# Kernel tuning notes

Hardware: AMD Instinct MI355X
Metric: run time of the kernel (lower is better)

Reference implementation:

```python
import jax, jax.numpy as jnp
import numpy as np

TEMPERATURE = 0.15
SINKHORN_ITERS = 5
CHUNKS = 8
DIM = 4096
CHUNK_SIZE = DIM // CHUNKS


def _sinkhorn(logits, num_iters=SINKHORN_ITERS):
    # Alternating row (dim=-1) then column (dim=-2) log-normalization, matching torch order.
    log_p = logits
    for _ in range(num_iters):
        log_p = log_p - jax.nn.logsumexp(log_p, axis=-1, keepdims=True)
        log_p = log_p - jax.nn.logsumexp(log_p, axis=-2, keepdims=True)
    return jnp.exp(log_p)


def setup_inputs() -> dict:
    key = jax.random.key(0)
    k1, k2, k3 = jax.random.split(key, 3)
    x = jax.random.normal(k1, (4, 4096, DIM), dtype=jnp.float32)
    chunk_logits = 0.01 * jax.random.normal(k2, (CHUNKS, CHUNKS), dtype=jnp.float32)
    intra_logits = 0.01 * jax.random.normal(k3, (CHUNKS, CHUNK_SIZE, CHUNK_SIZE), dtype=jnp.float32)
    return {"x": x, "chunk_logits": chunk_logits, "intra_logits": intra_logits}


def reference(x, chunk_logits, intra_logits):
    orig_shape = x.shape
    y = x.reshape(-1, CHUNKS, CHUNK_SIZE)  # [B, c, d]
    chunk_perm = _sinkhorn(chunk_logits / TEMPERATURE)  # [c, c]
    y = jnp.einsum('ij,bjd->bid', chunk_perm, y)
    intra_perm = _sinkhorn(intra_logits / TEMPERATURE)  # [c, d, d]
    # out[b,c,k] = sum_j y[b,c,j] * intra_perm[c,k,j]  (y @ intra_perm^T per chunk)
    y = jnp.einsum('bcj,ckj->bck', y, intra_perm)
    return y.reshape(orig_shape)
```

## Files before the change

kernel.cpp:

```cpp
#include <hip/hip_runtime.h>
#include <cstdint>
#include <cstddef>

typedef unsigned short u16;
typedef __bf16 bf16x8 __attribute__((ext_vector_type(8)));
typedef float f32x4 __attribute__((ext_vector_type(4)));
typedef u16 u16x8 __attribute__((ext_vector_type(8)));

typedef const void __attribute__((address_space(1)))* gas_ptr;
typedef void __attribute__((address_space(3)))* las_ptr;

#define TEMP_INV (1.0f / 0.15f)
#define NCH 8
#define CS 512
#define DIM 4096

__device__ __forceinline__ u16 f2bf(float f) {
  union { float f; uint32_t u; } a; a.f = f;
  uint32_t r = a.u + 0x7fffu + ((a.u >> 16) & 1u);
  return (u16)(r >> 16);
}

__device__ __forceinline__ float wave_sum(float s) {
  s += __shfl_xor(s, 1);  s += __shfl_xor(s, 2);  s += __shfl_xor(s, 4);
  s += __shfl_xor(s, 8);  s += __shfl_xor(s, 16); s += __shfl_xor(s, 32);
  return s;
}

__global__ __launch_bounds__(1024) void prep_kernel(
    const float* __restrict__ x,
    const float* __restrict__ chunk_logits,
    const float* __restrict__ intra_logits,
    u16* __restrict__ P,
    u16* __restrict__ Y)
{
  __shared__ float u_s[CS];
  __shared__ float v_s[CS];
  __shared__ float ps[8][CS];
  __shared__ float cps[64];

  const int bid = blockIdx.x;
  const int tid = threadIdx.x;

  if (bid < NCH) {
    const int c = bid;
    const int wv = tid >> 6, l = tid & 63;
    const float* Lc = intra_logits + (size_t)c * CS * CS;

    for (int r = wv; r < CS; r += 16) {
      const float* Lr = Lc + (size_t)r * CS;
      float s = 0.0f;
      #pragma unroll
      for (int rd = 0; rd < 2; ++rd) {
        const int j = rd * 256 + l * 4;
        float4 t = *(const float4*)(Lr + j);
        s += __expf(t.x * TEMP_INV) + __expf(t.y * TEMP_INV)
           + __expf(t.z * TEMP_INV) + __expf(t.w * TEMP_INV);
      }
      s = wave_sum(s);
      if (l == 0) u_s[r] = 1.0f / s;
    }
    __syncthreads();

    for (int it = 0; it < 5; ++it) {
      {
        const int cq = (tid & 127) * 4, slab = tid >> 7;
        const float* Ls = Lc + (size_t)slab * 64 * CS + cq;
        float ax = 0.f, ay = 0.f, az = 0.f, aw = 0.f;
        #pragma unroll 8
        for (int rr = 0; rr < 64; ++rr) {
          float4 t = *(const float4*)(Ls + (size_t)rr * CS);
          const float uu = u_s[slab * 64 + rr];
          ax += __expf(t.x * TEMP_INV) * uu;
          ay += __expf(t.y * TEMP_INV) * uu;
          az += __expf(t.z * TEMP_INV) * uu;
          aw += __expf(t.w * TEMP_INV) * uu;
        }
        float4 a; a.x = ax; a.y = ay; a.z = az; a.w = aw;
        *(float4*)&ps[slab][cq] = a;
      }
      __syncthreads();
      if (tid < CS) {
        float s = 0.0f;
        #pragma unroll
        for (int sl = 0; sl < 8; ++sl) s += ps[sl][tid];
        v_s[tid] = 1.0f / s;
      }
      __syncthreads();
      if (it == 4) break;
      for (int r = wv; r < CS; r += 16) {
        const float* Lr = Lc + (size_t)r * CS;
        float s = 0.0f;
        #pragma unroll
        for (int rd = 0; rd < 2; ++rd) {
          const int j = rd * 256 + l * 4;
          float4 t = *(const float4*)(Lr + j);
          float4 v = *(const float4*)(v_s + j);
          s += __expf(t.x * TEMP_INV) * v.x + __expf(t.y * TEMP_INV) * v.y
             + __expf(t.z * TEMP_INV) * v.z + __expf(t.w * TEMP_INV) * v.w;
        }
        s = wave_sum(s);
        if (l == 0) u_s[r] = 1.0f / s;
      }
      __syncthreads();
    }

    for (int r = wv; r < CS; r += 16) {
      const float uu = u_s[r];
      const float* Lr = Lc + (size_t)r * CS;
      u16* Pr = P + ((size_t)c * CS + r) * CS;
      const int j0 = l * 8;
      float4 t0 = *(const float4*)(Lr + j0);
      float4 t1 = *(const float4*)(Lr + j0 + 4);
      float4 v0 = *(const float4*)(v_s + j0);
      float4 v1 = *(const float4*)(v_s + j0 + 4);
      u16x8 o;
      o[0] = f2bf(__expf(t0.x * TEMP_INV) * uu * v0.x);
      o[1] = f2bf(__expf(t0.y * TEMP_INV) * uu * v0.y);
      o[2] = f2bf(__expf(t0.z * TEMP_INV) * uu * v0.z);
      o[3] = f2bf(__expf(t0.w * TEMP_INV) * uu * v0.w);
      o[4] = f2bf(__expf(t1.x * TEMP_INV) * uu * v1.x);
      o[5] = f2bf(__expf(t1.y * TEMP_INV) * uu * v1.y);
      o[6] = f2bf(__expf(t1.z * TEMP_INV) * uu * v1.z);
      o[7] = f2bf(__expf(t1.w * TEMP_INV) * uu * v1.w);
      *(u16x8*)(Pr + j0) = o;
    }
    return;
  }

  if (tid < 64) {
    float e = __expf(chunk_logits[tid] * TEMP_INV);
    float v = 1.0f, uu = 0.0f;
    #pragma unroll
    for (int it = 0; it < 5; ++it) {
      float t = e * v;
      t += __shfl_xor(t, 1); t += __shfl_xor(t, 2); t += __shfl_xor(t, 4);
      uu = 1.0f / t;
      float t2 = e * uu;
      t2 += __shfl_xor(t2, 8); t2 += __shfl_xor(t2, 16); t2 += __shfl_xor(t2, 32);
      v = 1.0f / t2;
    }
    cps[tid] = e * uu * v;
  }
  __syncthreads();

  const int g  = (bid - NCH) * 1024 + tid;
  const int b  = g >> 7;
  const int d4 = g & 127;

  const float4* xr = (const float4*)x + (size_t)b * 1024 + d4;
  float4 xi[8];
  #pragma unroll
  for (int jc = 0; jc < 8; ++jc) xi[jc] = xr[(size_t)jc * 128];

  ushort4* yr = (ushort4*)Y + (size_t)b * 1024 + d4;
  #pragma unroll
  for (int i = 0; i < 8; ++i) {
    float ax = 0.f, ay = 0.f, az = 0.f, aw = 0.f;
    #pragma unroll
    for (int jc = 0; jc < 8; ++jc) {
      const float wgt = cps[i * 8 + jc];
      ax += wgt * xi[jc].x; ay += wgt * xi[jc].y;
      az += wgt * xi[jc].z; aw += wgt * xi[jc].w;
    }
    ushort4 o;
    o.x = f2bf(ax); o.y = f2bf(ay); o.z = f2bf(az); o.w = f2bf(aw);
    yr[(size_t)i * 128] = o;
  }
}

#define BM 128
#define BN 128
#define BK 32
#define NT (CS / BK)

__global__ __launch_bounds__(256) void gemm_kernel(
    const u16* __restrict__ Y,
    const u16* __restrict__ P,
    float* __restrict__ out)
{
  __shared__ u16 As[2][BM * BK];
  __shared__ u16 Bs[2][BN * BK];

  const int tid = threadIdx.x;
  const int m0 = blockIdx.x * BM;
  const int n0 = blockIdx.y * BN;
  const int c  = blockIdx.z;

  const u16* Ab = Y + (size_t)m0 * DIM + (size_t)c * CS;
  const u16* Bb = P + ((size_t)c * CS + n0) * CS;

  const int w = tid >> 6, l = tid & 63;
  const int wm = (w >> 1) * 64, wn = (w & 1) * 64;
  const int lrow = l & 15, sub = l >> 4;

  f32x4 acc[4][4] = {};

  auto stage = [&](int buf, int kk) {
    #pragma unroll
    for (int rd = 0; rd < 2; ++rd) {
      const int idx = rd * 256 + tid;
      const int r = idx >> 2;
      const int cb = ((idx & 3) ^ (r & 3)) << 3;
      __builtin_amdgcn_global_load_lds((gas_ptr)(Ab + (size_t)r * DIM + kk + cb),
                                       (las_ptr)(&As[buf][(idx & ~63) * 8]), 16, 0, 0);
    }
    #pragma unroll
    for (int rd = 0; rd < 2; ++rd) {
      const int idx = rd * 256 + tid;
      const int r = idx >> 2;
      const int cb = ((idx & 3) ^ (r & 3)) << 3;
      __builtin_amdgcn_global_load_lds((gas_ptr)(Bb + (size_t)r * CS + kk + cb),
                                       (las_ptr)(&Bs[buf][(idx & ~63) * 8]), 16, 0, 0);
    }
  };

  stage(0, 0);
  __syncthreads();

  int cur = 0;
  for (int t = 0; t < NT; ++t) {
    if (t + 1 < NT) stage(cur ^ 1, (t + 1) * BK);

    bf16x8 yf[4], pf[4];
    #pragma unroll
    for (int mi = 0; mi < 4; ++mi) {
      const int row = wm + mi * 16 + lrow;
      yf[mi] = *(const bf16x8*)&As[cur][row * BK + ((sub ^ (row & 3)) << 3)];
    }
    #pragma unroll
    for (int ni = 0; ni < 4; ++ni) {
      const int row = wn + ni * 16 + lrow;
      pf[ni] = *(const bf16x8*)&Bs[cur][row * BK + ((sub ^ (row & 3)) << 3)];
    }

    #pragma unroll
    for (int mi = 0; mi < 4; ++mi)
      #pragma unroll
      for (int ni = 0; ni < 4; ++ni)
        acc[mi][ni] = __builtin_amdgcn_mfma_f32_16x16x32_bf16(
            pf[ni], yf[mi], acc[mi][ni], 0, 0, 0);

    __syncthreads();
    cur ^= 1;
  }

  const int nq = sub * 4;
  #pragma unroll
  for (int mi = 0; mi < 4; ++mi) {
    const size_t mrow = (size_t)(m0 + wm + mi * 16 + lrow) * DIM + (size_t)c * CS;
    #pragma unroll
    for (int ni = 0; ni < 4; ++ni) {
      __builtin_nontemporal_store(acc[mi][ni],
          (f32x4*)(out + mrow + (size_t)(n0 + wn + ni * 16 + nq)));
    }
  }
}

extern "C" void kernel_launch(void* const* d_in, const int* in_sizes, int n_in,
                              void* d_out, int out_size, void* d_ws, size_t ws_size,
                              hipStream_t stream) {
  const float* x  = (const float*)d_in[0];
  const float* cl = (const float*)d_in[1];
  const float* il = (const float*)d_in[2];
  float* out = (float*)d_out;

  char* ws = (char*)d_ws;
  u16* P = (u16*)ws;
  u16* Y = (u16*)(ws + (size_t)8 * 1024 * 1024);

  const int rows = in_sizes[0] / DIM;

  prep_kernel<<<dim3(NCH + rows / 8), dim3(1024), 0, stream>>>(x, cl, il, P, Y);
  gemm_kernel<<<dim3(rows / BM, CS / BN, NCH), dim3(256), 0, stream>>>(Y, P, out);
}
```

Measured before the change: 687.8 us.

## Split per-chunk Sinkhorn across 8 blocks with atomic column sums and grid barrier

Each chunk's 512x512 Sinkhorn normalization now runs on 8 cooperating blocks, each owning 64 rows, instead of one 1024-thread block. Column sums are combined through global atomicAdd into a workspace, and the blocks wait on a spin barrier built from per-iteration counters. The prep kernel block size drops to 256, and the chunk-mixing part of the grid is resized to match. This is meant to shorten the serial Sinkhorn critical path, which ran on only 8 blocks. In exchange it adds a memset launch, atomics, and a spin-wait that assumes all 64 Sinkhorn blocks are co-resident.

```diff
diff --git a/kernel.cpp b/kernel.cpp
--- a/kernel.cpp
+++ b/kernel.cpp
@@ -14,6 +14,7 @@
 #define NCH 8
 #define CS 512
 #define DIM 4096
+#define SINK_BLOCKS 64
 
 __device__ __forceinline__ u16 f2bf(float f) {
   union { float f; uint32_t u; } a; a.f = f;
@@ -27,88 +28,101 @@
   return s;
 }
 
-__global__ __launch_bounds__(1024) void prep_kernel(
+__global__ __launch_bounds__(256) void prep_kernel(
     const float* __restrict__ x,
     const float* __restrict__ chunk_logits,
     const float* __restrict__ intra_logits,
     u16* __restrict__ P,
-    u16* __restrict__ Y)
+    u16* __restrict__ Y,
+    float* __restrict__ vacc,
+    int* __restrict__ cnt)
 {
-  __shared__ float u_s[CS];
+  __shared__ float u_s[64];
   __shared__ float v_s[CS];
-  __shared__ float ps[8][CS];
+  __shared__ float ps2[2][CS];
   __shared__ float cps[64];
 
   const int bid = blockIdx.x;
   const int tid = threadIdx.x;
 
-  if (bid < NCH) {
-    const int c = bid;
+  if (bid < SINK_BLOCKS) {
+    const int c = bid >> 3, s = bid & 7;
     const int wv = tid >> 6, l = tid & 63;
-    const float* Lc = intra_logits + (size_t)c * CS * CS;
-
-    for (int r = wv; r < CS; r += 16) {
-      const float* Lr = Lc + (size_t)r * CS;
-      float s = 0.0f;
-      #pragma unroll
-      for (int rd = 0; rd < 2; ++rd) {
-        const int j = rd * 256 + l * 4;
-        float4 t = *(const float4*)(Lr + j);
-        s += __expf(t.x * TEMP_INV) + __expf(t.y * TEMP_INV)
-           + __expf(t.z * TEMP_INV) + __expf(t.w * TEMP_INV);
-      }
-      s = wave_sum(s);
-      if (l == 0) u_s[r] = 1.0f / s;
-    }
+    const float* Ls = intra_logits + ((size_t)c * CS + s * 64) * CS;
+    int* cnt_c = cnt + c * 5;
+
+    v_s[tid] = 1.0f; v_s[tid + 256] = 1.0f;
     __syncthreads();
 
-    for (int it = 0; it < 5; ++it) {
-      {
-        const int cq = (tid & 127) * 4, slab = tid >> 7;
-        const float* Ls = Lc + (size_t)slab * 64 * CS + cq;
-        float ax = 0.f, ay = 0.f, az = 0.f, aw = 0.f;
-        #pragma unroll 8
-        for (int rr = 0; rr < 64; ++rr) {
-          float4 t = *(const float4*)(Ls + (size_t)rr * CS);
-          const float uu = u_s[slab * 64 + rr];
-          ax += __expf(t.x * TEMP_INV) * uu;
-          ay += __expf(t.y * TEMP_INV) * uu;
-          az += __expf(t.z * TEMP_INV) * uu;
-          aw += __expf(t.w * TEMP_INV) * uu;
-        }
-        float4 a; a.x = ax; a.y = ay; a.z = az; a.w = aw;
-        *(float4*)&ps[slab][cq] = a;
-      }
-      __syncthreads();
-      if (tid < CS) {
-        float s = 0.0f;
-        #pragma unroll
-        for (int sl = 0; sl < 8; ++sl) s += ps[sl][tid];
-        v_s[tid] = 1.0f / s;
-      }
-      __syncthreads();
-      if (it == 4) break;
-      for (int r = wv; r < CS; r += 16) {
-        const float* Lr = Lc + (size_t)r * CS;
-        float s = 0.0f;
+    auto rowpass = [&]() {
+      for (int r = wv; r < 64; r += 4) {
+        const float* Lr = Ls + (size_t)r * CS;
+        float acc = 0.0f;
         #pragma unroll
         for (int rd = 0; rd < 2; ++rd) {
           const int j = rd * 256 + l * 4;
           float4 t = *(const float4*)(Lr + j);
           float4 v = *(const float4*)(v_s + j);
-          s += __expf(t.x * TEMP_INV) * v.x + __expf(t.y * TEMP_INV) * v.y
-             + __expf(t.z * TEMP_INV) * v.z + __expf(t.w * TEMP_INV) * v.w;
+          acc += __expf(t.x * TEMP_INV) * v.x + __expf(t.y * TEMP_INV) * v.y
+               + __expf(t.z * TEMP_INV) * v.z + __expf(t.w * TEMP_INV) * v.w;
         }
-        s = wave_sum(s);
-        if (l == 0) u_s[r] = 1.0f / s;
-      }
-      __syncthreads();
-    }
-
-    for (int r = wv; r < CS; r += 16) {
+        acc = wave_sum(acc);
+        if (l == 0) u_s[r] = 1.0f / acc;
+      }
+      __syncthreads();
+    };
+
+    rowpass();
+
+    for (int it = 0; it < 5; ++it) {
+      const int half = tid >> 7, ct = tid & 127;
+      const float* Lh = Ls + (size_t)half * 32 * CS + ct * 4;
+      float ax = 0.f, ay = 0.f, az = 0.f, aw = 0.f;
+      #pragma unroll 4
+      for (int rr = 0; rr < 32; ++rr) {
+        float4 t = *(const float4*)(Lh + (size_t)rr * CS);
+        const float uu = u_s[half * 32 + rr];
+        ax += __expf(t.x * TEMP_INV) * uu;
+        ay += __expf(t.y * TEMP_INV) * uu;
+        az += __expf(t.z * TEMP_INV) * uu;
+        aw += __expf(t.w * TEMP_INV) * uu;
+      }
+      float4 a; a.x = ax; a.y = ay; a.z = az; a.w = aw;
+      *(float4*)&ps2[half][ct * 4] = a;
+      __syncthreads();
+
+      float* va = vacc + ((size_t)it * NCH + c) * CS;
+      #pragma unroll
+      for (int rep = 0; rep < 2; ++rep) {
+        const int j = rep * 256 + tid;
+        atomicAdd(&va[j], ps2[0][j] + ps2[1][j]);
+      }
+      __syncthreads();
+
+      if (tid == 0) {
+        __hip_atomic_fetch_add(&cnt_c[it], 1, __ATOMIC_RELEASE,
+                               __HIP_MEMORY_SCOPE_AGENT);
+        while (__hip_atomic_load(&cnt_c[it], __ATOMIC_ACQUIRE,
+                                 __HIP_MEMORY_SCOPE_AGENT) < 8)
+          __builtin_amdgcn_s_sleep(2);
+      }
+      __syncthreads();
+
+      #pragma unroll
+      for (int rep = 0; rep < 2; ++rep) {
+        const int j = rep * 256 + tid;
+        v_s[j] = 1.0f / __hip_atomic_load(&va[j], __ATOMIC_RELAXED,
+                                          __HIP_MEMORY_SCOPE_AGENT);
+      }
+      __syncthreads();
+
+      if (it < 4) rowpass();
+    }
+
+    for (int r = wv; r < 64; r += 4) {
       const float uu = u_s[r];
-      const float* Lr = Lc + (size_t)r * CS;
-      u16* Pr = P + ((size_t)c * CS + r) * CS;
+      const float* Lr = Ls + (size_t)r * CS;
+      u16* Pr = P + ((size_t)c * CS + s * 64 + r) * CS;
       const int j0 = l * 8;
       float4 t0 = *(const float4*)(Lr + j0);
       float4 t1 = *(const float4*)(Lr + j0 + 4);
@@ -144,7 +158,7 @@
   }
   __syncthreads();
 
-  const int g  = (bid - NCH) * 1024 + tid;
+  const int g  = (bid - SINK_BLOCKS) * 256 + tid;
   const int b  = g >> 7;
   const int d4 = g & 127;
 
@@ -266,11 +280,15 @@
   float* out = (float*)d_out;
 
   char* ws = (char*)d_ws;
-  u16* P = (u16*)ws;
-  u16* Y = (u16*)(ws + (size_t)8 * 1024 * 1024);
+  u16*   P    = (u16*)ws;
+  float* vacc = (float*)(ws + (size_t)4 * 1024 * 1024);
+  int*   cnt  = (int*)(ws + (size_t)4 * 1024 * 1024 + 80 * 1024);
+  u16*   Y    = (u16*)(ws + (size_t)8 * 1024 * 1024);
 
   const int rows = in_sizes[0] / DIM;
 
-  prep_kernel<<<dim3(NCH + rows / 8), dim3(1024), 0, stream>>>(x, cl, il, P, Y);
+  hipMemsetAsync(ws + (size_t)4 * 1024 * 1024, 0, 80 * 1024 + 256, stream);
+  prep_kernel<<<dim3(SINK_BLOCKS + rows / 2), dim3(256), 0, stream>>>(
+      x, cl, il, P, Y, vacc, cnt);
   gemm_kernel<<<dim3(rows / BM, CS / BN, NCH), dim3(256), 0, stream>>>(Y, P, out);
 }
```

Result: faster. 626.8 us (-8.9%).
